# Kernel tuning notes

Hardware: AMD Instinct MI355X
Metric: run time of the kernel (lower is better)

The kernel has to match this reference:

```python
import jax, jax.numpy as jnp
import numpy as np

BN_EPS = 1e-5
NUM_GRAPHS = 64

def _bn(h, gamma, beta):
    # BatchNorm1d over node dim, training-mode (batch statistics, biased var)
    mu = jnp.mean(h, axis=0)
    var = jnp.mean(jnp.square(h - mu), axis=0)
    return gamma * (h - mu) * jax.lax.rsqrt(var + BN_EPS) + beta

def _gin_conv(x, src, dst, Wa, ba, gamma, beta, Wb, bb):
    # sum-aggregate neighbor features: agg[v] = sum_{(u,v) in E} x[u]
    n = x.shape[0]
    agg = jax.ops.segment_sum(x[src], dst, num_segments=n)
    h = x + agg  # eps = 0 (default GINConv)
    h = jax.nn.relu(_bn(h @ Wa + ba, gamma, beta))
    return jax.nn.relu(h @ Wb + bb)

def setup_inputs() -> dict:
    key = jax.random.key(0)
    ks = jax.random.split(key, 16)
    N, E, IN, D, OUT = 50000, 800000, 128, 512, 10
    x = jax.random.normal(ks[0], (N, IN), dtype=jnp.float32)
    edge_index = jax.random.randint(ks[1], (2, E), 0, N, dtype=jnp.int64)
    batch = jnp.sort(jax.random.randint(ks[2], (N,), 0, NUM_GRAPHS, dtype=jnp.int64))
    def lin(k, i, o):
        return jax.random.normal(k, (i, o), dtype=jnp.float32) / np.sqrt(i)
    return {
        "x": x, "edge_index": edge_index, "batch": batch,
        "W1a": lin(ks[3], IN, D), "b1a": jnp.zeros((D,), jnp.float32),
        "g1": jnp.ones((D,), jnp.float32), "be1": jnp.zeros((D,), jnp.float32),
        "W1b": lin(ks[4], D, D), "b1b": jnp.zeros((D,), jnp.float32),
        "W2a": lin(ks[5], D, D), "b2a": jnp.zeros((D,), jnp.float32),
        "g2": jnp.ones((D,), jnp.float32), "be2": jnp.zeros((D,), jnp.float32),
        "W2b": lin(ks[6], D, D), "b2b": jnp.zeros((D,), jnp.float32),
        "Wl1": lin(ks[7], D, D), "bl1": jnp.zeros((D,), jnp.float32),
        "Wl2": lin(ks[8], D, OUT), "bl2": jnp.zeros((OUT,), jnp.float32),
    }

def reference(x, edge_index, batch, W1a, b1a, g1, be1, W1b, b1b,
              W2a, b2a, g2, be2, W2b, b2b, Wl1, bl1, Wl2, bl2):
    src, dst = edge_index[0], edge_index[1]
    h = _gin_conv(x, src, dst, W1a, b1a, g1, be1, W1b, b1b)
    h = _gin_conv(h, src, dst, W2a, b2a, g2, be2, W2b, b2b)
    pooled = jax.ops.segment_sum(h, batch, num_segments=NUM_GRAPHS)  # [G, D]
    out = jax.nn.relu(pooled @ Wl1 + bl1)
    return out @ Wl2 + bl2  # [G, out_channels]
```

## Files before the change

kernel.cpp:

```cpp
#include <hip/hip_runtime.h>
#include <cstdint>
#include <cstddef>

#define N_NODES  50000
#define N_EDGES  800000
#define DIM_IN   128
#define DIM_H    512
#define N_GRAPHS 64
#define DIM_OUT  10
#define BN_EPS   1e-5f
#define SCAN_B   196

typedef _Float16 h16;
using f16x8 = __attribute__((ext_vector_type(8))) _Float16;
using f32x4 = __attribute__((ext_vector_type(4))) float;

__device__ inline float4 add4(float4 a, float4 b) {
    return make_float4(a.x + b.x, a.y + b.y, a.z + b.z, a.w + b.w);
}

__global__ __launch_bounds__(256) void k_wcast(
    const float* __restrict__ W, h16* __restrict__ Wt, int K, int N)
{
    int t = blockIdx.x * 256 + threadIdx.x;
    int total = (K >> 3) * N;
    if (t >= total) return;
    int k8 = t / N;
    int n  = t - k8 * N;
    f16x8 o;
#pragma unroll
    for (int j = 0; j < 8; ++j)
        o[j] = (h16)W[(size_t)(k8 * 8 + j) * N + n];
    *reinterpret_cast<f16x8*>(&Wt[(size_t)n * K + k8 * 8]) = o;
}

__global__ __launch_bounds__(256) void k_deg(
    const int* __restrict__ dst, int* __restrict__ deg)
{
    int t = blockIdx.x * 256 + threadIdx.x;
    if (t < N_EDGES) atomicAdd(&deg[dst[t]], 1);
}

__global__ __launch_bounds__(256) void k_scan1(
    const int* __restrict__ deg, int* __restrict__ bsum)
{
    __shared__ int s[256];
    int tid = threadIdx.x;
    int i = blockIdx.x * 256 + tid;
    s[tid] = (i < N_NODES) ? deg[i] : 0;
    __syncthreads();
    for (int off = 128; off > 0; off >>= 1) {
        if (tid < off) s[tid] += s[tid + off];
        __syncthreads();
    }
    if (tid == 0) bsum[blockIdx.x] = s[0];
}

__global__ __launch_bounds__(256) void k_scan2(
    const int* __restrict__ bsum, int* __restrict__ boff)
{
    __shared__ int s[256];
    int tid = threadIdx.x;
    s[tid] = (tid < SCAN_B) ? bsum[tid] : 0;
    __syncthreads();
    for (int off = 1; off < 256; off <<= 1) {
        int u = (tid >= off) ? s[tid - off] : 0;
        __syncthreads();
        s[tid] += u;
        __syncthreads();
    }
    if (tid < SCAN_B) boff[tid] = (tid == 0) ? 0 : s[tid - 1];
}

__global__ __launch_bounds__(256) void k_scan3(
    const int* __restrict__ deg, const int* __restrict__ boff,
    int* __restrict__ rowptr, int* __restrict__ cursor)
{
    __shared__ int s[256];
    int tid = threadIdx.x;
    int i = blockIdx.x * 256 + tid;
    int v = (i < N_NODES) ? deg[i] : 0;
    s[tid] = v;
    __syncthreads();
    for (int off = 1; off < 256; off <<= 1) {
        int u = (tid >= off) ? s[tid - off] : 0;
        __syncthreads();
        s[tid] += u;
        __syncthreads();
    }
    int excl = s[tid] - v + boff[blockIdx.x];
    if (i < N_NODES) {
        rowptr[i] = excl;
        cursor[i] = excl;
        if (i == N_NODES - 1) rowptr[N_NODES] = excl + v;
    }
}

__global__ __launch_bounds__(256) void k_fill(
    const int* __restrict__ src, const int* __restrict__ dst,
    int* __restrict__ cursor, int* __restrict__ eidx)
{
    int t = blockIdx.x * 256 + threadIdx.x;
    if (t >= N_EDGES) return;
    int pos = atomicAdd(&cursor[dst[t]], 1);
    eidx[pos] = src[t];
}

__global__ __launch_bounds__(256) void k_gather128(
    const float4* __restrict__ X, const int* __restrict__ rowptr,
    const int* __restrict__ eidx, f16x8* __restrict__ out)
{
    int t = blockIdx.x * 256 + threadIdx.x;
    int v = t >> 4, lane = t & 15;
    if (v >= N_NODES) return;
    int r0 = rowptr[v], r1 = rowptr[v + 1];
    float4 a0 = X[(size_t)v * 32 + lane * 2];
    float4 a1 = X[(size_t)v * 32 + lane * 2 + 1];
    for (int j = r0; j < r1; ++j) {
        int s = eidx[j];
        a0 = add4(a0, X[(size_t)s * 32 + lane * 2]);
        a1 = add4(a1, X[(size_t)s * 32 + lane * 2 + 1]);
    }
    f16x8 o;
    o[0] = (h16)a0.x; o[1] = (h16)a0.y; o[2] = (h16)a0.z; o[3] = (h16)a0.w;
    o[4] = (h16)a1.x; o[5] = (h16)a1.y; o[6] = (h16)a1.z; o[7] = (h16)a1.w;
    out[(size_t)v * 16 + lane] = o;
}

__global__ __launch_bounds__(256) void k_gather512h(
    const f16x8* __restrict__ X, const int* __restrict__ rowptr,
    const int* __restrict__ eidx, f16x8* __restrict__ out)
{
    int t = blockIdx.x * 256 + threadIdx.x;
    int v = t >> 6, lane = t & 63;
    if (v >= N_NODES) return;
    int r0 = rowptr[v], r1 = rowptr[v + 1];
    f16x8 sv = X[(size_t)v * 64 + lane];
    float a[8];
#pragma unroll
    for (int i = 0; i < 8; ++i) a[i] = (float)sv[i];
    int j = r0;
    for (; j + 3 < r1; j += 4) {
        int s0 = eidx[j], s1 = eidx[j + 1], s2 = eidx[j + 2], s3 = eidx[j + 3];
        f16x8 b0 = X[(size_t)s0 * 64 + lane];
        f16x8 b1 = X[(size_t)s1 * 64 + lane];
        f16x8 b2 = X[(size_t)s2 * 64 + lane];
        f16x8 b3 = X[(size_t)s3 * 64 + lane];
#pragma unroll
        for (int i = 0; i < 8; ++i)
            a[i] += ((float)b0[i] + (float)b1[i]) + ((float)b2[i] + (float)b3[i]);
    }
    for (; j < r1; ++j) {
        f16x8 b = X[(size_t)eidx[j] * 64 + lane];
#pragma unroll
        for (int i = 0; i < 8; ++i) a[i] += (float)b[i];
    }
    f16x8 o;
#pragma unroll
    for (int i = 0; i < 8; ++i) o[i] = (h16)a[i];
    out[(size_t)v * 64 + lane] = o;
}

template<bool AFFINE, bool RELU, bool STATS>
__global__ __launch_bounds__(512) void k_gemm_mfma(
    const h16* __restrict__ A, const h16* __restrict__ Bt,
    const float* __restrict__ bias, const float* __restrict__ sA,
    const float* __restrict__ cA, h16* __restrict__ C,
    float* __restrict__ csum, float* __restrict__ csq,
    int M, int N, int K, int lda)
{
    __shared__ h16 As[4][128][8];
    __shared__ h16 Bs[4][256][8];

    const int tid  = threadIdx.x;
    const int lane = tid & 63;
    const int w    = tid >> 6;
    const int wr   = w >> 2;
    const int wc   = w & 3;
    const int l15  = lane & 15;
    const int lk   = lane >> 4;
    const int m0   = blockIdx.x * 128;
    const int n0   = blockIdx.y * 256;

    const int s_row = tid >> 2;
    const int s_kb  = tid & 3;
    int ar = m0 + s_row; if (ar >= M) ar = M - 1;
    const h16* aptr = A + (size_t)ar * lda + s_kb * 8;
    const int b_kb0 = tid >> 8, b_nc0 = tid & 255;
    const int b_kb1 = (tid + 512) >> 8, b_nc1 = tid & 255;

    f32x4 acc[4][4];
#pragma unroll
    for (int m = 0; m < 4; ++m)
#pragma unroll
        for (int n = 0; n < 4; ++n)
            acc[m][n] = (f32x4){0.f, 0.f, 0.f, 0.f};

    for (int k0 = 0; k0 < K; k0 += 32) {
        f16x8 av = *reinterpret_cast<const f16x8*>(aptr + k0);
        if (AFFINE) {
            int kk = k0 + s_kb * 8;
            float4 s0 = *reinterpret_cast<const float4*>(&sA[kk]);
            float4 s1 = *reinterpret_cast<const float4*>(&sA[kk + 4]);
            float4 c0 = *reinterpret_cast<const float4*>(&cA[kk]);
            float4 c1 = *reinterpret_cast<const float4*>(&cA[kk + 4]);
            float va[8];
#pragma unroll
            for (int i = 0; i < 8; ++i) va[i] = (float)av[i];
            va[0] = fmaxf(fmaf(va[0], s0.x, c0.x), 0.f);
            va[1] = fmaxf(fmaf(va[1], s0.y, c0.y), 0.f);
            va[2] = fmaxf(fmaf(va[2], s0.z, c0.z), 0.f);
            va[3] = fmaxf(fmaf(va[3], s0.w, c0.w), 0.f);
            va[4] = fmaxf(fmaf(va[4], s1.x, c1.x), 0.f);
            va[5] = fmaxf(fmaf(va[5], s1.y, c1.y), 0.f);
            va[6] = fmaxf(fmaf(va[6], s1.z, c1.z), 0.f);
            va[7] = fmaxf(fmaf(va[7], s1.w, c1.w), 0.f);
#pragma unroll
            for (int i = 0; i < 8; ++i) av[i] = (h16)va[i];
        }
        f16x8 bw0 = *reinterpret_cast<const f16x8*>(
            &Bt[(size_t)(n0 + b_nc0) * K + k0 + b_kb0 * 8]);
        f16x8 bw1 = *reinterpret_cast<const f16x8*>(
            &Bt[(size_t)(n0 + b_nc1) * K + k0 + b_kb1 * 8]);

        __syncthreads();
        *reinterpret_cast<f16x8*>(&As[s_kb][s_row][0]) = av;
        *reinterpret_cast<f16x8*>(&Bs[b_kb0][b_nc0][0]) = bw0;
        *reinterpret_cast<f16x8*>(&Bs[b_kb1][b_nc1][0]) = bw1;
        __syncthreads();

        f16x8 af[4], bf[4];
#pragma unroll
        for (int m = 0; m < 4; ++m)
            af[m] = *reinterpret_cast<const f16x8*>(&As[lk][wr * 64 + m * 16 + l15][0]);
#pragma unroll
        for (int n = 0; n < 4; ++n)
            bf[n] = *reinterpret_cast<const f16x8*>(&Bs[lk][wc * 64 + n * 16 + l15][0]);
#pragma unroll
        for (int m = 0; m < 4; ++m)
#pragma unroll
            for (int n = 0; n < 4; ++n)
                acc[m][n] = __builtin_amdgcn_mfma_f32_16x16x32_f16(
                    af[m], bf[n], acc[m][n], 0, 0, 0);
    }

#pragma unroll
    for (int n = 0; n < 4; ++n) {
        int col = n0 + wc * 64 + n * 16 + l15;
        float bb = bias[col];
        float sp = 0.f, qp = 0.f;
#pragma unroll
        for (int m = 0; m < 4; ++m) {
            int row0 = m0 + wr * 64 + m * 16 + lk * 4;
#pragma unroll
            for (int r = 0; r < 4; ++r) {
                int row = row0 + r;
                if (row < M) {
                    float v = acc[m][n][r] + bb;
                    if (STATS) { sp += v; qp += v * v; }
                    if (RELU) v = fmaxf(v, 0.f);
                    C[(size_t)row * N + col] = (h16)v;
                }
            }
        }
        if (STATS) {
            sp += __shfl_xor(sp, 16); qp += __shfl_xor(qp, 16);
            sp += __shfl_xor(sp, 32); qp += __shfl_xor(qp, 32);
            if (lk == 0) {
                atomicAdd(&csum[col], sp);
                atomicAdd(&csq[col], qp);
            }
        }
    }
}

__global__ void k_fold(const float* __restrict__ csum, const float* __restrict__ csq,
                       const float* __restrict__ g, const float* __restrict__ be,
                       float* __restrict__ sf, float* __restrict__ cf)
{
    int c = threadIdx.x;
    const float invM = 1.0f / (float)N_NODES;
    float mu  = csum[c] * invM;
    float var = csq[c] * invM - mu * mu;
    float s   = g[c] * rsqrtf(var + BN_EPS);
    sf[c] = s;
    cf[c] = be[c] - mu * s;
}

__global__ __launch_bounds__(256) void k_pool(
    const h16* __restrict__ H, const int* __restrict__ batch,
    float* __restrict__ pooled)
{
    __shared__ int bg[128];
    int base = blockIdx.x * 128;
    if (threadIdx.x < 128) {
        int r = base + threadIdx.x;
        bg[threadIdx.x] = (r < N_NODES) ? batch[r] : -1;
    }
    __syncthreads();
    int c0 = threadIdx.x;
    float a0 = 0.f, a1 = 0.f;
    int cur = bg[0];
    for (int r = 0; r < 128; ++r) {
        int g = bg[r];
        if (g < 0) break;
        if (g != cur) {
            atomicAdd(&pooled[cur * DIM_H + c0],       a0);
            atomicAdd(&pooled[cur * DIM_H + c0 + 256], a1);
            a0 = a1 = 0.f;
            cur = g;
        }
        size_t row = (size_t)(base + r);
        a0 += (float)H[row * DIM_H + c0];
        a1 += (float)H[row * DIM_H + c0 + 256];
    }
    if (cur >= 0) {
        atomicAdd(&pooled[cur * DIM_H + c0],       a0);
        atomicAdd(&pooled[cur * DIM_H + c0 + 256], a1);
    }
}

__global__ __launch_bounds__(512) void k_head1(
    const float* __restrict__ pooled, const float* __restrict__ W,
    const float* __restrict__ b, float* __restrict__ q)
{
    __shared__ float row[DIM_H];
    int g = blockIdx.x, c = threadIdx.x;
    row[c] = pooled[(size_t)g * DIM_H + c];
    __syncthreads();
    float acc = 0.f;
    for (int k = 0; k < DIM_H; ++k)
        acc = fmaf(row[k], W[(size_t)k * DIM_H + c], acc);
    q[(size_t)g * DIM_H + c] = fmaxf(acc + b[c], 0.f);
}

__global__ __launch_bounds__(256) void k_head2(
    const float* __restrict__ q, const float* __restrict__ W,
    const float* __restrict__ b, float* __restrict__ out)
{
    int t = blockIdx.x * 256 + threadIdx.x;
    if (t >= N_GRAPHS * DIM_OUT) return;
    int g = t / DIM_OUT, c = t % DIM_OUT;
    float acc = 0.f;
    for (int k = 0; k < DIM_H; ++k)
        acc = fmaf(q[(size_t)g * DIM_H + k], W[(size_t)k * DIM_OUT + c], acc);
    out[t] = acc + b[c];
}

extern "C" void kernel_launch(void* const* d_in, const int* in_sizes, int n_in,
                              void* d_out, int out_size, void* d_ws, size_t ws_size,
                              hipStream_t stream)
{
    const float* x   = (const float*)d_in[0];
    const int*   ei  = (const int*)d_in[1];
    const int*   src = ei;
    const int*   dst = ei + N_EDGES;
    const int*   batch = (const int*)d_in[2];
    const float* W1a = (const float*)d_in[3];
    const float* b1a = (const float*)d_in[4];
    const float* g1  = (const float*)d_in[5];
    const float* be1 = (const float*)d_in[6];
    const float* W1b = (const float*)d_in[7];
    const float* b1b = (const float*)d_in[8];
    const float* W2a = (const float*)d_in[9];
    const float* b2a = (const float*)d_in[10];
    const float* g2  = (const float*)d_in[11];
    const float* be2 = (const float*)d_in[12];
    const float* W2b = (const float*)d_in[13];
    const float* b2b = (const float*)d_in[14];
    const float* Wl1 = (const float*)d_in[15];
    const float* bl1 = (const float*)d_in[16];
    const float* Wl2 = (const float*)d_in[17];
    const float* bl2 = (const float*)d_in[18];

    char* ws = (char*)d_ws;
    const size_t ROW_H = (size_t)N_NODES * DIM_H * 2;

    if (ws_size < 110000000ull) {
        hipMemsetAsync(d_out, 0, (size_t)out_size * 4, stream);
        return;
    }
    h16* B1h = (h16*)(ws + 0);
    h16* B2h = (h16*)(ws + ROW_H);
    h16* XAh = B2h;
    char* cp  = ws + 2 * ROW_H;
    int* deg    = (int*)(cp + 0);
    int* rowptr = (int*)(cp + 200192);
    int* cursor = (int*)(cp + 400384);
    int* eidx   = (int*)(cp + 600576);
    char* sm    = cp + 3800576;
    float* csum   = (float*)(sm + 0);
    float* csq    = (float*)(sm + 2048);
    float* sf     = (float*)(sm + 4096);
    float* cf     = (float*)(sm + 6144);
    float* pooled = (float*)(sm + 8192);
    float* qbuf   = (float*)(sm + 8192 + 131072);
    char* wt = sm + 8192 + 2 * 131072;
    h16* Wt1a = (h16*)(wt);
    h16* Wt1b = (h16*)(wt + 131072);
    h16* Wt2a = (h16*)(wt + 131072 + 524288);
    h16* Wt2b = (h16*)(wt + 131072 + 2 * 524288);
    int* bsum = (int*)(wt + 131072 + 3 * 524288);
    int* boff = bsum + 256;

    const dim3 gemm_grid(391, 2);
    const int EB = (N_EDGES + 255) / 256;

    k_wcast<<<32, 256, 0, stream>>>(W1a, Wt1a, DIM_IN, DIM_H);
    k_wcast<<<128, 256, 0, stream>>>(W1b, Wt1b, DIM_H, DIM_H);
    k_wcast<<<128, 256, 0, stream>>>(W2a, Wt2a, DIM_H, DIM_H);
    k_wcast<<<128, 256, 0, stream>>>(W2b, Wt2b, DIM_H, DIM_H);

    hipMemsetAsync(deg, 0, (size_t)N_NODES * 4, stream);
    k_deg<<<EB, 256, 0, stream>>>(dst, deg);
    k_scan1<<<SCAN_B, 256, 0, stream>>>(deg, bsum);
    k_scan2<<<1, 256, 0, stream>>>(bsum, boff);
    k_scan3<<<SCAN_B, 256, 0, stream>>>(deg, boff, rowptr, cursor);
    k_fill<<<EB, 256, 0, stream>>>(src, dst, cursor, eidx);

    k_gather128<<<(N_NODES * 16 + 255) / 256, 256, 0, stream>>>(
        (const float4*)x, rowptr, eidx, (f16x8*)XAh);
    hipMemsetAsync(csum, 0, 4096, stream);
    k_gemm_mfma<false, false, true><<<gemm_grid, 512, 0, stream>>>(
        XAh, Wt1a, b1a, nullptr, nullptr, B1h, csum, csq,
        N_NODES, DIM_H, DIM_IN, DIM_IN);
    k_fold<<<1, 512, 0, stream>>>(csum, csq, g1, be1, sf, cf);
    k_gemm_mfma<true, true, false><<<gemm_grid, 512, 0, stream>>>(
        B1h, Wt1b, b1b, sf, cf, B2h, nullptr, nullptr,
        N_NODES, DIM_H, DIM_H, DIM_H);

    k_gather512h<<<(N_NODES * 64) / 256, 256, 0, stream>>>(
        (const f16x8*)B2h, rowptr, eidx, (f16x8*)B1h);
    hipMemsetAsync(csum, 0, 4096, stream);
    k_gemm_mfma<false, false, true><<<gemm_grid, 512, 0, stream>>>(
        B1h, Wt2a, b2a, nullptr, nullptr, B2h, csum, csq,
        N_NODES, DIM_H, DIM_H, DIM_H);
    k_fold<<<1, 512, 0, stream>>>(csum, csq, g2, be2, sf, cf);
    k_gemm_mfma<true, true, false><<<gemm_grid, 512, 0, stream>>>(
        B2h, Wt2b, b2b, sf, cf, B1h, nullptr, nullptr,
        N_NODES, DIM_H, DIM_H, DIM_H);

    hipMemsetAsync(pooled, 0, (size_t)N_GRAPHS * DIM_H * 4, stream);
    k_pool<<<(N_NODES + 127) / 128, 256, 0, stream>>>(B1h, batch, pooled);
    k_head1<<<N_GRAPHS, 512, 0, stream>>>(pooled, Wl1, bl1, qbuf);
    k_head2<<<3, 256, 0, stream>>>(qbuf, Wl2, bl2, (float*)d_out);
}
```

Before: 691.2 us.

## Double K-tile to 64 with register prefetch in GEMM; unroll gather by 8

The MFMA GEMM now stages a 64-wide K slice per iteration instead of 32, which halves the number of barrier pairs. It also prefetches the next tile's global loads into registers before running the MFMAs on the current tile, so load latency overlaps with compute. Separately, the neighbor gather loop is unrolled to 8 edges with a 2-edge and a 1-edge tail, giving more memory-level parallelism. The cost is a larger shared-memory footprint and more live registers, which may lower occupancy. The GEMM now assumes K is a multiple of 64.

```diff
diff --git a/kernel.cpp b/kernel.cpp
--- a/kernel.cpp
+++ b/kernel.cpp
@@ -140,17 +140,27 @@
 #pragma unroll
     for (int i = 0; i < 8; ++i) a[i] = (float)sv[i];
     int j = r0;
-    for (; j + 3 < r1; j += 4) {
-        int s0 = eidx[j], s1 = eidx[j + 1], s2 = eidx[j + 2], s3 = eidx[j + 3];
-        f16x8 b0 = X[(size_t)s0 * 64 + lane];
-        f16x8 b1 = X[(size_t)s1 * 64 + lane];
-        f16x8 b2 = X[(size_t)s2 * 64 + lane];
-        f16x8 b3 = X[(size_t)s3 * 64 + lane];
+    for (; j + 7 < r1; j += 8) {
+        f16x8 b0 = X[(size_t)eidx[j]     * 64 + lane];
+        f16x8 b1 = X[(size_t)eidx[j + 1] * 64 + lane];
+        f16x8 b2 = X[(size_t)eidx[j + 2] * 64 + lane];
+        f16x8 b3 = X[(size_t)eidx[j + 3] * 64 + lane];
+        f16x8 b4 = X[(size_t)eidx[j + 4] * 64 + lane];
+        f16x8 b5 = X[(size_t)eidx[j + 5] * 64 + lane];
+        f16x8 b6 = X[(size_t)eidx[j + 6] * 64 + lane];
+        f16x8 b7 = X[(size_t)eidx[j + 7] * 64 + lane];
 #pragma unroll
         for (int i = 0; i < 8; ++i)
-            a[i] += ((float)b0[i] + (float)b1[i]) + ((float)b2[i] + (float)b3[i]);
-    }
-    for (; j < r1; ++j) {
+            a[i] += (((float)b0[i] + (float)b1[i]) + ((float)b2[i] + (float)b3[i]))
+                  + (((float)b4[i] + (float)b5[i]) + ((float)b6[i] + (float)b7[i]));
+    }
+    for (; j + 1 < r1; j += 2) {
+        f16x8 b0 = X[(size_t)eidx[j]     * 64 + lane];
+        f16x8 b1 = X[(size_t)eidx[j + 1] * 64 + lane];
+#pragma unroll
+        for (int i = 0; i < 8; ++i) a[i] += (float)b0[i] + (float)b1[i];
+    }
+    if (j < r1) {
         f16x8 b = X[(size_t)eidx[j] * 64 + lane];
 #pragma unroll
         for (int i = 0; i < 8; ++i) a[i] += (float)b[i];
@@ -169,8 +179,8 @@
     float* __restrict__ csum, float* __restrict__ csq,
     int M, int N, int K, int lda)
 {
-    __shared__ h16 As[4][128][8];
-    __shared__ h16 Bs[4][256][8];
+    __shared__ h16 As[8][128][8];
+    __shared__ h16 Bs[8][256][8];
 
     const int tid  = threadIdx.x;
     const int lane = tid & 63;
@@ -182,12 +192,15 @@
     const int m0   = blockIdx.x * 128;
     const int n0   = blockIdx.y * 256;
 
-    const int s_row = tid >> 2;
-    const int s_kb  = tid & 3;
-    int ar = m0 + s_row; if (ar >= M) ar = M - 1;
-    const h16* aptr = A + (size_t)ar * lda + s_kb * 8;
-    const int b_kb0 = tid >> 8, b_nc0 = tid & 255;
-    const int b_kb1 = (tid + 512) >> 8, b_nc1 = tid & 255;
+    const int a_row0 = tid >> 3;
+    const int kb     = tid & 7;
+    int ar0 = m0 + a_row0;      if (ar0 >= M) ar0 = M - 1;
+    int ar1 = m0 + a_row0 + 64; if (ar1 >= M) ar1 = M - 1;
+    const h16* aptr0 = A + (size_t)ar0 * lda + kb * 8;
+    const h16* aptr1 = A + (size_t)ar1 * lda + kb * 8;
+    const int b_col0 = tid >> 3;
+    const h16* bptr = Bt + (size_t)(n0 + b_col0) * K + kb * 8;
+    const size_t bstride = (size_t)64 * K;
 
     f32x4 acc[4][4];
 #pragma unroll
@@ -196,52 +209,63 @@
         for (int n = 0; n < 4; ++n)
             acc[m][n] = (f32x4){0.f, 0.f, 0.f, 0.f};
 
-    for (int k0 = 0; k0 < K; k0 += 32) {
-        f16x8 av = *reinterpret_cast<const f16x8*>(aptr + k0);
+    f16x8 av0, av1, bw0, bw1, bw2, bw3;
+
+    auto load_tile = [&](int k0) {
+        av0 = *reinterpret_cast<const f16x8*>(aptr0 + k0);
+        av1 = *reinterpret_cast<const f16x8*>(aptr1 + k0);
         if (AFFINE) {
-            int kk = k0 + s_kb * 8;
+            int kk = k0 + kb * 8;
             float4 s0 = *reinterpret_cast<const float4*>(&sA[kk]);
             float4 s1 = *reinterpret_cast<const float4*>(&sA[kk + 4]);
             float4 c0 = *reinterpret_cast<const float4*>(&cA[kk]);
             float4 c1 = *reinterpret_cast<const float4*>(&cA[kk + 4]);
-            float va[8];
-#pragma unroll
-            for (int i = 0; i < 8; ++i) va[i] = (float)av[i];
-            va[0] = fmaxf(fmaf(va[0], s0.x, c0.x), 0.f);
-            va[1] = fmaxf(fmaf(va[1], s0.y, c0.y), 0.f);
-            va[2] = fmaxf(fmaf(va[2], s0.z, c0.z), 0.f);
-            va[3] = fmaxf(fmaf(va[3], s0.w, c0.w), 0.f);
-            va[4] = fmaxf(fmaf(va[4], s1.x, c1.x), 0.f);
-            va[5] = fmaxf(fmaf(va[5], s1.y, c1.y), 0.f);
-            va[6] = fmaxf(fmaf(va[6], s1.z, c1.z), 0.f);
-            va[7] = fmaxf(fmaf(va[7], s1.w, c1.w), 0.f);
-#pragma unroll
-            for (int i = 0; i < 8; ++i) av[i] = (h16)va[i];
+            float sarr[8] = {s0.x, s0.y, s0.z, s0.w, s1.x, s1.y, s1.z, s1.w};
+            float carr[8] = {c0.x, c0.y, c0.z, c0.w, c1.x, c1.y, c1.z, c1.w};
+#pragma unroll
+            for (int i = 0; i < 8; ++i) {
+                av0[i] = (h16)fmaxf(fmaf((float)av0[i], sarr[i], carr[i]), 0.f);
+                av1[i] = (h16)fmaxf(fmaf((float)av1[i], sarr[i], carr[i]), 0.f);
+            }
         }
-        f16x8 bw0 = *reinterpret_cast<const f16x8*>(
-            &Bt[(size_t)(n0 + b_nc0) * K + k0 + b_kb0 * 8]);
-        f16x8 bw1 = *reinterpret_cast<const f16x8*>(
-            &Bt[(size_t)(n0 + b_nc1) * K + k0 + b_kb1 * 8]);
-
-        __syncthreads();
-        *reinterpret_cast<f16x8*>(&As[s_kb][s_row][0]) = av;
-        *reinterpret_cast<f16x8*>(&Bs[b_kb0][b_nc0][0]) = bw0;
-        *reinterpret_cast<f16x8*>(&Bs[b_kb1][b_nc1][0]) = bw1;
-        __syncthreads();
-
-        f16x8 af[4], bf[4];
-#pragma unroll
-        for (int m = 0; m < 4; ++m)
-            af[m] = *reinterpret_cast<const f16x8*>(&As[lk][wr * 64 + m * 16 + l15][0]);
-#pragma unroll
-        for (int n = 0; n < 4; ++n)
-            bf[n] = *reinterpret_cast<const f16x8*>(&Bs[lk][wc * 64 + n * 16 + l15][0]);
-#pragma unroll
-        for (int m = 0; m < 4; ++m)
+        bw0 = *reinterpret_cast<const f16x8*>(bptr + k0);
+        bw1 = *reinterpret_cast<const f16x8*>(bptr + bstride + k0);
+        bw2 = *reinterpret_cast<const f16x8*>(bptr + 2 * bstride + k0);
+        bw3 = *reinterpret_cast<const f16x8*>(bptr + 3 * bstride + k0);
+    };
+
+    load_tile(0);
+
+    for (int k0 = 0; k0 < K; k0 += 64) {
+        __syncthreads();
+        *reinterpret_cast<f16x8*>(&As[kb][a_row0][0])        = av0;
+        *reinterpret_cast<f16x8*>(&As[kb][a_row0 + 64][0])   = av1;
+        *reinterpret_cast<f16x8*>(&Bs[kb][b_col0][0])        = bw0;
+        *reinterpret_cast<f16x8*>(&Bs[kb][b_col0 + 64][0])   = bw1;
+        *reinterpret_cast<f16x8*>(&Bs[kb][b_col0 + 128][0])  = bw2;
+        *reinterpret_cast<f16x8*>(&Bs[kb][b_col0 + 192][0])  = bw3;
+        __syncthreads();
+
+        if (k0 + 64 < K) load_tile(k0 + 64);
+
+#pragma unroll
+        for (int s = 0; s < 2; ++s) {
+            f16x8 af[4], bf[4];
+#pragma unroll
+            for (int m = 0; m < 4; ++m)
+                af[m] = *reinterpret_cast<const f16x8*>(
+                    &As[s * 4 + lk][wr * 64 + m * 16 + l15][0]);
 #pragma unroll
             for (int n = 0; n < 4; ++n)
-                acc[m][n] = __builtin_amdgcn_mfma_f32_16x16x32_f16(
-                    af[m], bf[n], acc[m][n], 0, 0, 0);
+                bf[n] = *reinterpret_cast<const f16x8*>(
+                    &Bs[s * 4 + lk][wc * 64 + n * 16 + l15][0]);
+#pragma unroll
+            for (int m = 0; m < 4; ++m)
+#pragma unroll
+                for (int n = 0; n < 4; ++n)
+                    acc[m][n] = __builtin_amdgcn_mfma_f32_16x16x32_f16(
+                        af[m], bf[n], acc[m][n], 0, 0, 0);
+        }
     }
 
 #pragma unroll
```

Result: slower. 813.1 us (+17.6%).
